# Performance work log

Measured on AMD Instinct MI355X. Metric: run time of the kernel, lower is better.

## Reference

```python
import jax, jax.numpy as jnp
import numpy as np

NUM_GRAPHS = 128
NODES_PER_GRAPH = 512
NUM_NODES = NUM_GRAPHS * NODES_PER_GRAPH
NUM_EDGES = NUM_NODES * 16
IN_DIM = 64
HID = 128
NUM_HEADS = 4
BN_EPS = 1e-5


def setup_inputs() -> dict:
    key = jax.random.key(0)
    ks = jax.random.split(key, 12)
    x = jax.random.normal(ks[0], (NUM_NODES, IN_DIM), dtype=jnp.float32)
    edge_index = jax.random.randint(ks[1], (2, NUM_EDGES), 0, NUM_NODES, dtype=jnp.int32)
    batch = jnp.repeat(jnp.arange(NUM_GRAPHS, dtype=jnp.int32), NODES_PER_GRAPH)
    s = 0.05
    W0 = jax.random.normal(ks[2], (IN_DIM, HID), dtype=jnp.float32) * s
    b0 = jnp.zeros((HID,), jnp.float32)
    Wh = jax.random.normal(ks[3], (3, HID, HID), dtype=jnp.float32) * s  # convs 1..3
    bh = jnp.zeros((3, HID), jnp.float32)
    bn_gamma = jnp.ones((4, HID), jnp.float32)
    bn_beta = jnp.zeros((4, HID), jnp.float32)
    bn_mean = jnp.zeros((4, HID), jnp.float32)
    bn_var = jnp.ones((4, HID), jnp.float32)
    attn_in_w = jax.random.normal(ks[4], (3 * HID, HID), dtype=jnp.float32) * s
    attn_in_b = jnp.zeros((3 * HID,), jnp.float32)
    attn_out_w = jax.random.normal(ks[5], (HID, HID), dtype=jnp.float32) * s
    attn_out_b = jnp.zeros((HID,), jnp.float32)
    return dict(x=x, W0=W0, b0=b0, Wh=Wh, bh=bh, bn_gamma=bn_gamma, bn_beta=bn_beta,
                bn_mean=bn_mean, bn_var=bn_var, attn_in_w=attn_in_w, attn_in_b=attn_in_b,
                attn_out_w=attn_out_w, attn_out_b=attn_out_b, edge_index=edge_index, batch=batch)


def _forward(x, W0, b0, Wh, bh, bn_gamma, bn_beta, bn_mean, bn_var,
             attn_in_w, attn_in_b, attn_out_w, attn_out_b, edge_index, batch):
    N = x.shape[0]
    src, dst = edge_index[0], edge_index[1]
    # GCN symmetric normalization with self-loops (PyG GCNConv)
    deg = jax.ops.segment_sum(jnp.ones_like(src, jnp.float32), dst, num_segments=N) + 1.0
    dis = jax.lax.rsqrt(deg)                      # deg^{-1/2}
    enorm = (dis[src] * dis[dst])[:, None]        # per-edge norm
    self_norm = (dis * dis)[:, None]              # self-loop norm

    def gcn(h, W, b):
        h = h @ W
        agg = jax.ops.segment_sum(h[src] * enorm, dst, num_segments=N)
        return agg + h * self_norm + b

    def bn(h, i):
        scale = bn_gamma[i] * jax.lax.rsqrt(bn_var[i] + BN_EPS)
        return (h - bn_mean[i]) * scale + bn_beta[i]  # eval-mode BN

    # dropout is identity in eval mode
    h = jax.nn.relu(bn(gcn(x, W0, b0), 0))
    h = jax.nn.relu(bn(gcn(h, Wh[0], bh[0]), 1))
    h = jax.nn.relu(bn(gcn(h, Wh[1], bh[1]), 2))
    f = jax.nn.relu(bn(gcn(h, Wh[2], bh[2]), 3))   # [N, HID]

    # per-graph self-attention (equal-size contiguous graphs -> batched MHA)
    dh = HID // NUM_HEADS
    xg = f.reshape(NUM_GRAPHS, NODES_PER_GRAPH, HID)
    qkv = xg @ attn_in_w.T + attn_in_b            # [G, n, 3H]
    q, k, v = jnp.split(qkv, 3, axis=-1)

    def heads(t):
        return t.reshape(NUM_GRAPHS, NODES_PER_GRAPH, NUM_HEADS, dh).transpose(0, 2, 1, 3)
    q, k, v = heads(q), heads(k), heads(v)
    scores = jnp.einsum('ghnd,ghmd->ghnm', q, k) / np.sqrt(dh).astype(np.float32)
    attn = jax.nn.softmax(scores, axis=-1)
    o = jnp.einsum('ghnm,ghmd->ghnd', attn, v).transpose(0, 2, 1, 3).reshape(NUM_GRAPHS, NODES_PER_GRAPH, HID)
    o = o @ attn_out_w.T + attn_out_b
    final = o.reshape(N, HID)

    # global mean pool over batch indices
    cnt = jax.ops.segment_sum(jnp.ones((N,), jnp.float32), batch, num_segments=NUM_GRAPHS)
    graph_emb = jax.ops.segment_sum(final, batch, num_segments=NUM_GRAPHS) / cnt[:, None]
    return final, graph_emb


def reference(x, W0, b0, Wh, bh, bn_gamma, bn_beta, bn_mean, bn_var,
              attn_in_w, attn_in_b, attn_out_w, attn_out_b, edge_index, batch):
    return _forward(x, W0, b0, Wh, bh, bn_gamma, bn_beta, bn_mean, bn_var,
                    attn_in_w, attn_in_b, attn_out_w, attn_out_b, edge_index, batch)
```

## Files before the change

### kernel.cpp

```cpp
#include <hip/hip_runtime.h>
#include <hip/hip_bf16.h>
#include <cstdint>
#include <cstddef>

#define N_NODES 65536
#define N_EDGES 1048576
#define N_GRAPHS 128
#define NPG 512
#define IN_DIM 64
#define HID 128
#define BN_EPS 1e-5f

typedef __attribute__((ext_vector_type(8))) short bf16x8;
typedef __attribute__((ext_vector_type(4))) float f32x4;
typedef __attribute__((ext_vector_type(8))) unsigned short u16x8;
typedef __attribute__((ext_vector_type(4))) unsigned int u32x4;

__device__ inline unsigned short f2bf(float f) {
  unsigned u = __builtin_bit_cast(unsigned, f);
  u = u + 0x7fffu + ((u >> 16) & 1u);
  return (unsigned short)(u >> 16);
}
__device__ inline float bf2f(unsigned short h) {
  unsigned u = ((unsigned)h) << 16;
  return __builtin_bit_cast(float, u);
}
__device__ inline void split_bf(float v, unsigned short& hi, unsigned short& lo) {
  hi = f2bf(v);
  lo = f2bf(v - bf2f(hi));
}
__device__ inline void split_bf_fast(float v, unsigned short& hi, unsigned short& lo) {
  unsigned u = __builtin_bit_cast(unsigned, v);
  hi = (unsigned short)(u >> 16);
  float r = v - __builtin_bit_cast(float, u & 0xffff0000u);
  lo = f2bf(r);
}

__global__ __launch_bounds__(256) void hist_kernel(const int* __restrict__ dst,
                                                   int* __restrict__ deg) {
  int e = blockIdx.x * 256 + threadIdx.x;
  if (e < N_EDGES) atomicAdd(&deg[dst[e]], 1);
}

__global__ __launch_bounds__(256) void dis_kernel(const int* __restrict__ deg,
                                                  float* __restrict__ dis) {
  int n = blockIdx.x * 256 + threadIdx.x;
  if (n < N_NODES) dis[n] = 1.0f / sqrtf((float)deg[n] + 1.0f);
}

__global__ __launch_bounds__(1024) void scan_kernel(const int* __restrict__ deg,
                                                    int* __restrict__ offsets,
                                                    int* __restrict__ cursor) {
  __shared__ int sums[1024];
  int t = threadIdx.x;
  int base = t * 64;
  const int4* dp = (const int4*)(deg + base);
  int s = 0;
#pragma unroll
  for (int i = 0; i < 16; i++) {
    int4 v = dp[i];
    s += v.x + v.y + v.z + v.w;
  }
  sums[t] = s;
  __syncthreads();
  for (int off = 1; off < 1024; off <<= 1) {
    int v = (t >= off) ? sums[t - off] : 0;
    __syncthreads();
    sums[t] += v;
    __syncthreads();
  }
  int run = (t == 0) ? 0 : sums[t - 1];
#pragma unroll
  for (int i = 0; i < 16; i++) {
    int4 v = dp[i];
    int idx = base + i * 4;
    offsets[idx] = run; cursor[idx] = run; run += v.x;
    offsets[idx + 1] = run; cursor[idx + 1] = run; run += v.y;
    offsets[idx + 2] = run; cursor[idx + 2] = run; run += v.z;
    offsets[idx + 3] = run; cursor[idx + 3] = run; run += v.w;
  }
  if (t == 1023) offsets[N_NODES] = run;
}

__global__ __launch_bounds__(256) void fill_kernel(const int* __restrict__ src,
                                                   const int* __restrict__ dst,
                                                   int* __restrict__ cursor,
                                                   int* __restrict__ csr) {
  int e = blockIdx.x * 256 + threadIdx.x;
  if (e < N_EDGES) {
    int d = dst[e];
    int slot = atomicAdd(&cursor[d], 1);
    csr[slot] = src[e];
  }
}

__global__ __launch_bounds__(256) void agg64_kernel(const float* __restrict__ x,
                                                    const float* __restrict__ dis,
                                                    const int* __restrict__ offsets,
                                                    const int* __restrict__ csr,
                                                    unsigned short* __restrict__ zhi,
                                                    unsigned short* __restrict__ zlo) {
  int node = blockIdx.x * 4 + (threadIdx.x >> 6);
  int lane = threadIdx.x & 63;
  float dn = dis[node];
  float acc = x[(size_t)node * 64 + lane] * dn * dn;
  int beg = offsets[node], end = offsets[node + 1];
  int k = beg;
  for (; k + 4 <= end; k += 4) {
    int s0 = csr[k], s1 = csr[k + 1], s2 = csr[k + 2], s3 = csr[k + 3];
    float w0 = dn * dis[s0], w1 = dn * dis[s1], w2 = dn * dis[s2], w3 = dn * dis[s3];
    float v0 = x[(size_t)s0 * 64 + lane];
    float v1 = x[(size_t)s1 * 64 + lane];
    float v2 = x[(size_t)s2 * 64 + lane];
    float v3 = x[(size_t)s3 * 64 + lane];
    acc = fmaf(w0, v0, acc);
    acc = fmaf(w1, v1, acc);
    acc = fmaf(w2, v2, acc);
    acc = fmaf(w3, v3, acc);
  }
  for (; k < end; k++) {
    int s = csr[k];
    acc = fmaf(dn * dis[s], x[(size_t)s * 64 + lane], acc);
  }
  unsigned short h_, l_;
  split_bf(acc, h_, l_);
  zhi[(size_t)node * 64 + lane] = h_;
  zlo[(size_t)node * 64 + lane] = l_;
}

__global__ __launch_bounds__(256) void agg128_kernel(const float* __restrict__ h,
                                                     const float* __restrict__ dis,
                                                     const int* __restrict__ offsets,
                                                     const int* __restrict__ csr,
                                                     unsigned short* __restrict__ zhi,
                                                     unsigned short* __restrict__ zlo) {
  int node = blockIdx.x * 4 + (threadIdx.x >> 6);
  int lane = threadIdx.x & 63;
  float dn = dis[node];
  float sn = dn * dn;
  const float* hr = h + (size_t)node * 128;
  float a0 = hr[lane] * sn;
  float a1 = hr[lane + 64] * sn;
  int beg = offsets[node], end = offsets[node + 1];
  int k = beg;
  for (; k + 4 <= end; k += 4) {
    int s0 = csr[k], s1 = csr[k + 1], s2 = csr[k + 2], s3 = csr[k + 3];
    float w0 = dn * dis[s0], w1 = dn * dis[s1], w2 = dn * dis[s2], w3 = dn * dis[s3];
    const float* p0 = h + (size_t)s0 * 128;
    const float* p1 = h + (size_t)s1 * 128;
    const float* p2 = h + (size_t)s2 * 128;
    const float* p3 = h + (size_t)s3 * 128;
    float u0 = p0[lane], d0 = p0[lane + 64];
    float u1 = p1[lane], d1 = p1[lane + 64];
    float u2 = p2[lane], d2 = p2[lane + 64];
    float u3 = p3[lane], d3 = p3[lane + 64];
    a0 = fmaf(w0, u0, a0); a1 = fmaf(w0, d0, a1);
    a0 = fmaf(w1, u1, a0); a1 = fmaf(w1, d1, a1);
    a0 = fmaf(w2, u2, a0); a1 = fmaf(w2, d2, a1);
    a0 = fmaf(w3, u3, a0); a1 = fmaf(w3, d3, a1);
  }
  for (; k < end; k++) {
    int s = csr[k];
    float w = dn * dis[s];
    const float* hs = h + (size_t)s * 128;
    a0 = fmaf(w, hs[lane], a0);
    a1 = fmaf(w, hs[lane + 64], a1);
  }
  unsigned short h0, l0, h1, l1;
  split_bf(a0, h0, l0);
  split_bf(a1, h1, l1);
  zhi[(size_t)node * 128 + lane] = h0;
  zlo[(size_t)node * 128 + lane] = l0;
  zhi[(size_t)node * 128 + lane + 64] = h1;
  zlo[(size_t)node * 128 + lane + 64] = l1;
}

template <bool TRANS>
__global__ __launch_bounds__(256) void wprep_kernel(const float* __restrict__ W, int K, int O,
                                                    unsigned short* __restrict__ hi,
                                                    unsigned short* __restrict__ lo) {
  int idx = blockIdx.x * 256 + threadIdx.x;
  int KC = K / 32;
  int total = (O / 16) * KC * 64;
  if (idx >= total) return;
  int lane = idx & 63;
  int rest = idx >> 6;
  int kc = rest % KC;
  int nt = rest / KC;
  int n = nt * 16 + (lane & 15);
  int kb = kc * 32 + (lane >> 4) * 8;
  unsigned short* hp = hi + (size_t)idx * 8;
  unsigned short* lp = lo + (size_t)idx * 8;
#pragma unroll
  for (int j = 0; j < 8; j++) {
    int k = kb + j;
    float v = TRANS ? W[(size_t)n * K + k] : W[(size_t)k * O + n];
    unsigned short h_, l_;
    split_bf(v, h_, l_);
    hp[j] = h_;
    lp[j] = l_;
  }
}

template <int K, int O, bool DOBN, bool DORELU, bool SPLIT_OUT, bool GROUPED,
          bool DOPOOL = false>
__global__ __launch_bounds__(256) void gemm_mfma(
    const unsigned short* __restrict__ Ahi, const unsigned short* __restrict__ Alo,
    const unsigned short* __restrict__ Whi, const unsigned short* __restrict__ Wlo,
    const float* __restrict__ bias,
    const float* __restrict__ gamma, const float* __restrict__ beta,
    const float* __restrict__ mean, const float* __restrict__ var,
    float* __restrict__ Cf, unsigned short* __restrict__ Chi,
    unsigned short* __restrict__ Clo, float* __restrict__ Pool = nullptr) {
  constexpr int KC = K / 32;
  int wave = threadIdx.x >> 6;
  int lane = threadIdx.x & 63;
  int m0 = blockIdx.x * 128 + wave * 32;
  int o0 = blockIdx.y * 128;
  int mrow = lane & 15;
  int kseg = (lane >> 4) * 8;

  f32x4 acc[2][8];
#pragma unroll
  for (int mt = 0; mt < 2; mt++)
#pragma unroll
    for (int nt = 0; nt < 8; nt++) acc[mt][nt] = (f32x4)0.0f;

#pragma unroll
  for (int kc = 0; kc < KC; kc++) {
    bf16x8 ah[2], al[2];
#pragma unroll
    for (int mt = 0; mt < 2; mt++) {
      size_t aoff = (size_t)(m0 + mt * 16 + mrow) * K + kc * 32 + kseg;
      ah[mt] = *(const bf16x8*)(Ahi + aoff);
      al[mt] = *(const bf16x8*)(Alo + aoff);
    }
#pragma unroll
    for (int nt = 0; nt < 8; nt++) {
      size_t foff = (((size_t)(blockIdx.y * 8 + nt) * KC + kc) * 64 + lane) * 8;
      bf16x8 bh = *(const bf16x8*)(Whi + foff);
      bf16x8 bl = *(const bf16x8*)(Wlo + foff);
#pragma unroll
      for (int mt = 0; mt < 2; mt++) {
        acc[mt][nt] = __builtin_amdgcn_mfma_f32_16x16x32_bf16(ah[mt], bh, acc[mt][nt], 0, 0, 0);
        acc[mt][nt] = __builtin_amdgcn_mfma_f32_16x16x32_bf16(ah[mt], bl, acc[mt][nt], 0, 0, 0);
        acc[mt][nt] = __builtin_amdgcn_mfma_f32_16x16x32_bf16(al[mt], bh, acc[mt][nt], 0, 0, 0);
        acc[mt][nt] = __builtin_amdgcn_mfma_f32_16x16x32_bf16(al[mt], bl, acc[mt][nt], 0, 0, 0);
      }
    }
  }

  int ccol = lane & 15;
  int crow0 = (lane >> 4) * 4;
  float colsum[8];
  if constexpr (DOPOOL) {
#pragma unroll
    for (int nt = 0; nt < 8; nt++) colsum[nt] = 0.0f;
  }
#pragma unroll
  for (int nt = 0; nt < 8; nt++) {
    int c = o0 + nt * 16 + ccol;
    float sc, cb;
    float b = bias[c];
    if (DOBN) {
      sc = gamma[c] * rsqrtf(var[c] + BN_EPS);
      cb = (b - mean[c]) * sc + beta[c];
    } else {
      sc = 1.0f;
      cb = b;
    }
#pragma unroll
    for (int mt = 0; mt < 2; mt++) {
#pragma unroll
      for (int r = 0; r < 4; r++) {
        float v = fmaf(acc[mt][nt][r], sc, cb);
        if (DORELU) v = fmaxf(v, 0.0f);
        size_t row = (size_t)(m0 + mt * 16 + crow0 + r);
        if (SPLIT_OUT) {
          unsigned short h_, l_;
          split_bf(v, h_, l_);
          if (GROUPED) {
            size_t base = row * (size_t)(2 * O) + (size_t)(((c >> 5) << 6) + (c & 31));
            Chi[base] = h_;
            Chi[base + 32] = l_;
          } else {
            Chi[row * O + c] = h_;
            Clo[row * O + c] = l_;
          }
        } else {
          Cf[row * O + c] = v;
        }
        if constexpr (DOPOOL) colsum[nt] += v;
      }
    }
  }
  if constexpr (DOPOOL) {
    __shared__ float pb[4][128];
#pragma unroll
    for (int nt = 0; nt < 8; nt++) {
      float cs = colsum[nt];
      cs += __shfl_xor(cs, 16, 64);
      cs += __shfl_xor(cs, 32, 64);
      if ((lane >> 4) == 0) pb[wave][nt * 16 + ccol] = cs;
    }
    __syncthreads();
    int tt = threadIdx.x;
    if (tt < 128) {
      float s2 = pb[0][tt] + pb[1][tt] + pb[2][tt] + pb[3][tt];
      int gg = blockIdx.x >> 2;
      atomicAdd(&Pool[gg * 128 + tt], s2 * (1.0f / NPG));
    }
  }
}

__global__ __launch_bounds__(256) void knorm_kernel(const unsigned short* __restrict__ qvs,
                                                    float* __restrict__ kmax2) {
  int g = blockIdx.x >> 2;
  int h = blockIdx.x & 3;
  size_t gbase = (size_t)g * NPG;
  float best = 0.0f;
#pragma unroll
  for (int r = 0; r < 2; r++) {
    int j = r * 256 + threadIdx.x;
    size_t base = (gbase + j) * 768 + (size_t)(4 + h) * 64;
    float s = 0.0f;
#pragma unroll
    for (int i = 0; i < 4; i++) {
      u16x8 hh = *(const u16x8*)(qvs + base + i * 8);
      u16x8 ll = *(const u16x8*)(qvs + base + 32 + i * 8);
#pragma unroll
      for (int jj = 0; jj < 8; jj++) {
        float v = bf2f(hh[jj]) + bf2f(ll[jj]);
        s = fmaf(v, v, s);
      }
    }
    best = fmaxf(best, s);
  }
#pragma unroll
  for (int off = 32; off >= 1; off >>= 1)
    best = fmaxf(best, __shfl_xor(best, off, 64));
  __shared__ float red[4];
  int wave = threadIdx.x >> 6;
  if ((threadIdx.x & 63) == 0) red[wave] = best;
  __syncthreads();
  if (threadIdx.x == 0) {
    float m = fmaxf(fmaxf(red[0], red[1]), fmaxf(red[2], red[3]));
    kmax2[blockIdx.x] = m;
  }
}

__global__ __launch_bounds__(256, 2) void attn_mfma_kernel(
    const unsigned short* __restrict__ qvs, const float* __restrict__ kmax2,
    unsigned short* __restrict__ ohi, unsigned short* __restrict__ olo) {
  int wb = ((blockIdx.x & 7) << 7) | (blockIdx.x >> 3);
  int g = wb >> 3;
  int h = (wb >> 1) & 3;
  int half = wb & 1;
  int t = threadIdx.x;
  int wave = t >> 6;
  int lane = t & 63;
  int quad = lane >> 4;
  int l15 = lane & 15;
  size_t gbase = (size_t)g * NPG;
  int qb = half * 256 + wave * 64;

  const float cf = 0.17677669529663687f * 1.4426950408889634f;

  __shared__ unsigned short Kh[2][32][40] __attribute__((aligned(16)));
  __shared__ unsigned short Kl[2][32][40] __attribute__((aligned(16)));
  __shared__ unsigned short Vh[2][33][40] __attribute__((aligned(16)));
  __shared__ unsigned short Vl[2][33][40] __attribute__((aligned(16)));
  __shared__ float Ot[64 * 36] __attribute__((aligned(16)));

  bf16x8 qh[4], ql[4];
  float Mq[4];
  float km2 = kmax2[g * 4 + h];
#pragma unroll
  for (int mt = 0; mt < 4; mt++) {
    size_t qoff = (gbase + qb + mt * 16 + l15) * 768 + (size_t)h * 64 + quad * 8;
    u16x8 hh = *(const u16x8*)(qvs + qoff);
    u16x8 ll = *(const u16x8*)(qvs + qoff + 32);
    qh[mt] = __builtin_bit_cast(bf16x8, hh);
    ql[mt] = __builtin_bit_cast(bf16x8, ll);
    float s = 0.0f;
#pragma unroll
    for (int j = 0; j < 8; j++) {
      float v = bf2f(hh[j]) + bf2f(ll[j]);
      s = fmaf(v, v, s);
    }
    s += __shfl_xor(s, 16);
    s += __shfl_xor(s, 32);
    Mq[mt] = cf * sqrtf(s * km2);
  }

  f32x4 Oa[4][3];
#pragma unroll
  for (int mt = 0; mt < 4; mt++)
#pragma unroll
    for (int nt = 0; nt < 3; nt++) Oa[mt][nt] = (f32x4)0.0f;

  if (t >= 64 && t < 72) {
    int u = t - 64;
    int bsel = u >> 2;
    int i = u & 3;
    u16x8 ones;
#pragma unroll
    for (int j = 0; j < 8; j++) ones[j] = 0x3F80;
    *(u16x8*)&Vh[bsel][32][i * 8] = ones;
  }

  bool isK = (t >= 128);
  bool isV = (t < 64);
  u16x8 kreg_h, kreg_l;
  ushort4 vreg_h[4], vreg_l[4];
  int kkey = 0, kds = 0, kphys = 0, vkeyb = 0, vdvb = 0;
  if (isK) {
    int t2 = t - 128;
    kkey = t2 >> 2;
    kds = (t2 & 3) * 8;
    int nt_ = kkey >> 4, q_ = (kkey >> 2) & 3, r_ = kkey & 3;
    int p_ = (nt_ << 1) | (r_ >> 1);
    kphys = 8 * (q_ ^ p_) + 2 * p_ + (r_ & 1);
  } else if (isV) {
    vkeyb = (t & 7) * 4;
    vdvb = (t >> 3) * 4;
  }

  auto load_chunk = [&](int c) {
    if (isK) {
      size_t ko = (gbase + (size_t)(c * 32 + kphys)) * 768 + (size_t)(4 + h) * 64 + kds;
      kreg_h = *(const u16x8*)(qvs + ko);
      kreg_l = *(const u16x8*)(qvs + ko + 32);
    } else if (isV) {
#pragma unroll
      for (int r = 0; r < 4; r++) {
        size_t vo = (gbase + (size_t)(c * 32 + vkeyb + r)) * 768 + (size_t)(8 + h) * 64 + vdvb;
        vreg_h[r] = *(const ushort4*)(qvs + vo);
        vreg_l[r] = *(const ushort4*)(qvs + vo + 32);
      }
    }
  };

  auto stage_chunk = [&](int bsel) {
    if (isK) {
      *(u16x8*)&Kh[bsel][kkey][kds] = kreg_h;
      *(u16x8*)&Kl[bsel][kkey][kds] = kreg_l;
    } else if (isV) {
      unsigned short ha[4][4], la[4][4];
#pragma unroll
      for (int r = 0; r < 4; r++) {
        *(ushort4*)&ha[r][0] = vreg_h[r];
        *(ushort4*)&la[r][0] = vreg_l[r];
      }
#pragma unroll
      for (int c2 = 0; c2 < 4; c2++) {
        ushort4 hv, lv;
        hv.x = ha[0][c2]; hv.y = ha[1][c2]; hv.z = ha[2][c2]; hv.w = ha[3][c2];
        lv.x = la[0][c2]; lv.y = la[1][c2]; lv.z = la[2][c2]; lv.w = la[3][c2];
        *(ushort4*)&Vh[bsel][vdvb + c2][vkeyb] = hv;
        *(ushort4*)&Vl[bsel][vdvb + c2][vkeyb] = lv;
      }
    }
  };

  load_chunk(0);
  stage_chunk(0);
  __syncthreads();

  int p = 0;
  for (int c = 0; c < 16; c++) {
    if (c < 15) load_chunk(c + 1);

    bf16x8 akh[2], akl[2];
    akh[0] = *(const bf16x8*)&Kh[p][l15][quad * 8];
    akh[1] = *(const bf16x8*)&Kh[p][16 + l15][quad * 8];
    akl[0] = *(const bf16x8*)&Kl[p][l15][quad * 8];
    akl[1] = *(const bf16x8*)&Kl[p][16 + l15][quad * 8];
    bf16x8 bvh0 = *(const bf16x8*)&Vh[p][l15][quad * 8];
    bf16x8 bvl0 = *(const bf16x8*)&Vl[p][l15][quad * 8];
    bf16x8 bvh1 = *(const bf16x8*)&Vh[p][16 + l15][quad * 8];
    bf16x8 bvl1 = *(const bf16x8*)&Vl[p][16 + l15][quad * 8];
    bf16x8 bvh2 = *(const bf16x8*)&Vh[p][32 + l15][quad * 8];

#pragma unroll
    for (int mt = 0; mt < 4; mt++) {
      unsigned pkh[4], pkl[4];
#pragma unroll
      for (int nt = 0; nt < 2; nt++) {
        f32x4 S = (f32x4)0.0f;
        S = __builtin_amdgcn_mfma_f32_16x16x32_bf16(akh[nt], qh[mt], S, 0, 0, 0);
        S = __builtin_amdgcn_mfma_f32_16x16x32_bf16(akh[nt], ql[mt], S, 0, 0, 0);
        S = __builtin_amdgcn_mfma_f32_16x16x32_bf16(akl[nt], qh[mt], S, 0, 0, 0);
        S = __builtin_amdgcn_mfma_f32_16x16x32_bf16(akl[nt], ql[mt], S, 0, 0, 0);
        unsigned short h0, l0, h1, l1, h2, l2, h3, l3;
        split_bf_fast(__builtin_exp2f(fmaf(S[0], cf, -Mq[mt])), h0, l0);
        split_bf_fast(__builtin_exp2f(fmaf(S[1], cf, -Mq[mt])), h1, l1);
        split_bf_fast(__builtin_exp2f(fmaf(S[2], cf, -Mq[mt])), h2, l2);
        split_bf_fast(__builtin_exp2f(fmaf(S[3], cf, -Mq[mt])), h3, l3);
        pkh[nt * 2]     = (unsigned)h0 | ((unsigned)h1 << 16);
        pkh[nt * 2 + 1] = (unsigned)h2 | ((unsigned)h3 << 16);
        pkl[nt * 2]     = (unsigned)l0 | ((unsigned)l1 << 16);
        pkl[nt * 2 + 1] = (unsigned)l2 | ((unsigned)l3 << 16);
      }
      u32x4 uh, ul;
      uh[0] = pkh[0];
      uh[1] = (unsigned)__shfl_xor((int)pkh[1], 16, 64);
      uh[2] = (unsigned)__shfl_xor((int)pkh[2], 32, 64);
      uh[3] = (unsigned)__shfl_xor((int)pkh[3], 48, 64);
      ul[0] = pkl[0];
      ul[1] = (unsigned)__shfl_xor((int)pkl[1], 16, 64);
      ul[2] = (unsigned)__shfl_xor((int)pkl[2], 32, 64);
      ul[3] = (unsigned)__shfl_xor((int)pkl[3], 48, 64);
      bf16x8 pa_h = __builtin_bit_cast(bf16x8, uh);
      bf16x8 pa_l = __builtin_bit_cast(bf16x8, ul);

      Oa[mt][0] = __builtin_amdgcn_mfma_f32_16x16x32_bf16(pa_h, bvh0, Oa[mt][0], 0, 0, 0);
      Oa[mt][0] = __builtin_amdgcn_mfma_f32_16x16x32_bf16(pa_h, bvl0, Oa[mt][0], 0, 0, 0);
      Oa[mt][0] = __builtin_amdgcn_mfma_f32_16x16x32_bf16(pa_l, bvh0, Oa[mt][0], 0, 0, 0);
      Oa[mt][1] = __builtin_amdgcn_mfma_f32_16x16x32_bf16(pa_h, bvh1, Oa[mt][1], 0, 0, 0);
      Oa[mt][1] = __builtin_amdgcn_mfma_f32_16x16x32_bf16(pa_h, bvl1, Oa[mt][1], 0, 0, 0);
      Oa[mt][1] = __builtin_amdgcn_mfma_f32_16x16x32_bf16(pa_l, bvh1, Oa[mt][1], 0, 0, 0);
      Oa[mt][2] = __builtin_amdgcn_mfma_f32_16x16x32_bf16(pa_h, bvh2, Oa[mt][2], 0, 0, 0);
      Oa[mt][2] = __builtin_amdgcn_mfma_f32_16x16x32_bf16(pa_l, bvh2, Oa[mt][2], 0, 0, 0);
    }

    if (c < 15) stage_chunk(p ^ 1);
    __syncthreads();
    p ^= 1;
  }

  for (int w = 0; w < 4; w++) {
    if (wave == w) {
#pragma unroll
      for (int mt = 0; mt < 4; mt++) {
#pragma unroll
        for (int r = 0; r < 4; r++) {
          int row = mt * 16 + quad * 4 + r;
          Ot[row * 36 + l15] = Oa[mt][0][r];
          Ot[row * 36 + 16 + l15] = Oa[mt][1][r];
          if (l15 == 0) Ot[row * 36 + 32] = Oa[mt][2][r];
        }
      }
      int row = lane;
      float inv = 1.0f / Ot[row * 36 + 32];
      size_t node = gbase + qb + row;
      u16x8 vh, vl;
#pragma unroll
      for (int seg = 0; seg < 4; seg++) {
#pragma unroll
        for (int j = 0; j < 8; j++) {
          unsigned short hi_, lo_;
          split_bf_fast(Ot[row * 36 + seg * 8 + j] * inv, hi_, lo_);
          vh[j] = hi_;
          vl[j] = lo_;
        }
        *(u16x8*)(ohi + node * 128 + h * 32 + seg * 8) = vh;
        *(u16x8*)(olo + node * 128 + h * 32 + seg * 8) = vl;
      }
    }
    __syncthreads();
  }
}

extern "C" void kernel_launch(void* const* d_in, const int* in_sizes, int n_in,
                              void* d_out, int out_size, void* d_ws, size_t ws_size,
                              hipStream_t stream) {
  (void)in_sizes; (void)n_in; (void)out_size; (void)ws_size;
  const float* x          = (const float*)d_in[0];
  const float* W0         = (const float*)d_in[1];
  const float* b0         = (const float*)d_in[2];
  const float* Wh         = (const float*)d_in[3];
  const float* bh         = (const float*)d_in[4];
  const float* bn_gamma   = (const float*)d_in[5];
  const float* bn_beta    = (const float*)d_in[6];
  const float* bn_mean    = (const float*)d_in[7];
  const float* bn_var     = (const float*)d_in[8];
  const float* attn_in_w  = (const float*)d_in[9];
  const float* attn_in_b  = (const float*)d_in[10];
  const float* attn_out_w = (const float*)d_in[11];
  const float* attn_out_b = (const float*)d_in[12];
  const int* edge_index   = (const int*)d_in[13];
  const int* src = edge_index;
  const int* dst = edge_index + N_EDGES;

  char* ws = (char*)d_ws;
  size_t off = 0;
  auto alloc = [&](size_t bytes) -> void* {
    void* p = ws + off;
    off += (bytes + 255) & ~(size_t)255;
    return p;
  };
  int*   deg     = (int*)alloc((size_t)N_NODES * 4);
  int*   offsets = (int*)alloc((size_t)(N_NODES + 1) * 4);
  int*   cursor  = (int*)alloc((size_t)N_NODES * 4);
  int*   csr     = (int*)alloc((size_t)N_EDGES * 4);
  float* dis     = (float*)alloc((size_t)N_NODES * 4);
  float* bufA    = (float*)alloc((size_t)N_NODES * HID * 4);
  unsigned short* zhi = (unsigned short*)alloc((size_t)N_NODES * HID * 2);
  unsigned short* zlo = (unsigned short*)alloc((size_t)N_NODES * HID * 2);
  unsigned short* qvs = (unsigned short*)alloc((size_t)N_NODES * 768 * 2);
  float* kmax2   = (float*)alloc((size_t)N_GRAPHS * 4 * 4);
  unsigned short* w0h = (unsigned short*)alloc(8192 * 2);
  unsigned short* w0l = (unsigned short*)alloc(8192 * 2);
  unsigned short* whh[3], *whl[3];
  for (int i = 0; i < 3; i++) {
    whh[i] = (unsigned short*)alloc(16384 * 2);
    whl[i] = (unsigned short*)alloc(16384 * 2);
  }
  unsigned short* wqh = (unsigned short*)alloc(49152 * 2);
  unsigned short* wql = (unsigned short*)alloc(49152 * 2);
  unsigned short* woh = (unsigned short*)alloc(16384 * 2);
  unsigned short* wol = (unsigned short*)alloc(16384 * 2);

  unsigned short* fhi = (unsigned short*)bufA;
  unsigned short* flo = fhi + (size_t)N_NODES * HID;

  float* fin = (float*)d_out;
  float* emb = fin + (size_t)N_NODES * HID;

  hipMemsetAsync(deg, 0, (size_t)N_NODES * 4, stream);
  hipMemsetAsync(emb, 0, (size_t)N_GRAPHS * HID * 4, stream);
  hist_kernel<<<N_EDGES / 256, 256, 0, stream>>>(dst, deg);
  dis_kernel<<<N_NODES / 256, 256, 0, stream>>>(deg, dis);
  scan_kernel<<<1, 1024, 0, stream>>>(deg, offsets, cursor);
  fill_kernel<<<N_EDGES / 256, 256, 0, stream>>>(src, dst, cursor, csr);

  wprep_kernel<false><<<4, 256, 0, stream>>>(W0, 64, 128, w0h, w0l);
  for (int i = 0; i < 3; i++)
    wprep_kernel<false><<<8, 256, 0, stream>>>(Wh + (size_t)i * HID * HID, 128, 128,
                                               whh[i], whl[i]);
  wprep_kernel<true><<<24, 256, 0, stream>>>(attn_in_w, 128, 384, wqh, wql);
  wprep_kernel<true><<<8, 256, 0, stream>>>(attn_out_w, 128, 128, woh, wol);

  dim3 ggrid(N_NODES / 128, 1);
  agg64_kernel<<<N_NODES / 4, 256, 0, stream>>>(x, dis, offsets, csr, zhi, zlo);
  gemm_mfma<64, 128, true, true, false, false><<<ggrid, 256, 0, stream>>>(
      zhi, zlo, w0h, w0l, b0, bn_gamma, bn_beta, bn_mean, bn_var, bufA, nullptr, nullptr);
  for (int L = 0; L < 2; L++) {
    agg128_kernel<<<N_NODES / 4, 256, 0, stream>>>(bufA, dis, offsets, csr, zhi, zlo);
    gemm_mfma<128, 128, true, true, false, false><<<ggrid, 256, 0, stream>>>(
        zhi, zlo, whh[L], whl[L], bh + (size_t)L * HID,
        bn_gamma + (size_t)(L + 1) * HID, bn_beta + (size_t)(L + 1) * HID,
        bn_mean + (size_t)(L + 1) * HID, bn_var + (size_t)(L + 1) * HID,
        bufA, nullptr, nullptr);
  }
  agg128_kernel<<<N_NODES / 4, 256, 0, stream>>>(bufA, dis, offsets, csr, zhi, zlo);
  gemm_mfma<128, 128, true, true, true, false><<<ggrid, 256, 0, stream>>>(
      zhi, zlo, whh[2], whl[2], bh + (size_t)2 * HID,
      bn_gamma + (size_t)3 * HID, bn_beta + (size_t)3 * HID,
      bn_mean + (size_t)3 * HID, bn_var + (size_t)3 * HID,
      nullptr, fhi, flo);
  dim3 qgrid(N_NODES / 128, 3);
  gemm_mfma<128, 384, false, false, true, true><<<qgrid, 256, 0, stream>>>(
      fhi, flo, wqh, wql, attn_in_b, nullptr, nullptr, nullptr, nullptr,
      nullptr, qvs, nullptr);
  knorm_kernel<<<N_GRAPHS * 4, 256, 0, stream>>>(qvs, kmax2);
  attn_mfma_kernel<<<N_GRAPHS * 4 * 2, 256, 0, stream>>>(qvs, kmax2, zhi, zlo);
  gemm_mfma<128, 128, false, false, false, false, true><<<ggrid, 256, 0, stream>>>(
      zhi, zlo, woh, wol, attn_out_b, nullptr, nullptr, nullptr, nullptr,
      fin, nullptr, nullptr, emb);
}
```

Measured before the change: 806.2 us.

## Unroll edge gathers by eight, use packed bf16 converts, precompute chunk pointers

```diff
diff --git a/kernel.cpp b/kernel.cpp
--- a/kernel.cpp
+++ b/kernel.cpp
@@ -34,6 +34,17 @@
   hi = (unsigned short)(u >> 16);
   float r = v - __builtin_bit_cast(float, u & 0xffff0000u);
   lo = f2bf(r);
+}
+__device__ inline unsigned cvt_pk_bf16(float a, float b) {
+  unsigned r;
+  asm("v_cvt_pk_bf16_f32 %0, %1, %2" : "=v"(r) : "v"(a), "v"(b));
+  return r;
+}
+__device__ inline void split2_pk(float a, float b, unsigned& hpk, unsigned& lpk) {
+  hpk = cvt_pk_bf16(a, b);
+  float ha = __builtin_bit_cast(float, hpk << 16);
+  float hb = __builtin_bit_cast(float, hpk & 0xffff0000u);
+  lpk = cvt_pk_bf16(a - ha, b - hb);
 }
 
 __global__ __launch_bounds__(256) void hist_kernel(const int* __restrict__ dst,
@@ -106,17 +117,18 @@
   float acc = x[(size_t)node * 64 + lane] * dn * dn;
   int beg = offsets[node], end = offsets[node + 1];
   int k = beg;
-  for (; k + 4 <= end; k += 4) {
-    int s0 = csr[k], s1 = csr[k + 1], s2 = csr[k + 2], s3 = csr[k + 3];
-    float w0 = dn * dis[s0], w1 = dn * dis[s1], w2 = dn * dis[s2], w3 = dn * dis[s3];
-    float v0 = x[(size_t)s0 * 64 + lane];
-    float v1 = x[(size_t)s1 * 64 + lane];
-    float v2 = x[(size_t)s2 * 64 + lane];
-    float v3 = x[(size_t)s3 * 64 + lane];
-    acc = fmaf(w0, v0, acc);
-    acc = fmaf(w1, v1, acc);
-    acc = fmaf(w2, v2, acc);
-    acc = fmaf(w3, v3, acc);
+  for (; k + 8 <= end; k += 8) {
+    int s[8];
+#pragma unroll
+    for (int i = 0; i < 8; i++) s[i] = csr[k + i];
+    float w[8];
+#pragma unroll
+    for (int i = 0; i < 8; i++) w[i] = dn * dis[s[i]];
+    float v[8];
+#pragma unroll
+    for (int i = 0; i < 8; i++) v[i] = x[(size_t)s[i] * 64 + lane];
+#pragma unroll
+    for (int i = 0; i < 8; i++) acc = fmaf(w[i], v[i], acc);
   }
   for (; k < end; k++) {
     int s = csr[k];
@@ -143,21 +155,25 @@
   float a1 = hr[lane + 64] * sn;
   int beg = offsets[node], end = offsets[node + 1];
   int k = beg;
-  for (; k + 4 <= end; k += 4) {
-    int s0 = csr[k], s1 = csr[k + 1], s2 = csr[k + 2], s3 = csr[k + 3];
-    float w0 = dn * dis[s0], w1 = dn * dis[s1], w2 = dn * dis[s2], w3 = dn * dis[s3];
-    const float* p0 = h + (size_t)s0 * 128;
-    const float* p1 = h + (size_t)s1 * 128;
-    const float* p2 = h + (size_t)s2 * 128;
-    const float* p3 = h + (size_t)s3 * 128;
-    float u0 = p0[lane], d0 = p0[lane + 64];
-    float u1 = p1[lane], d1 = p1[lane + 64];
-    float u2 = p2[lane], d2 = p2[lane + 64];
-    float u3 = p3[lane], d3 = p3[lane + 64];
-    a0 = fmaf(w0, u0, a0); a1 = fmaf(w0, d0, a1);
-    a0 = fmaf(w1, u1, a0); a1 = fmaf(w1, d1, a1);
-    a0 = fmaf(w2, u2, a0); a1 = fmaf(w2, d2, a1);
-    a0 = fmaf(w3, u3, a0); a1 = fmaf(w3, d3, a1);
+  for (; k + 8 <= end; k += 8) {
+    int s[8];
+#pragma unroll
+    for (int i = 0; i < 8; i++) s[i] = csr[k + i];
+    float w[8];
+#pragma unroll
+    for (int i = 0; i < 8; i++) w[i] = dn * dis[s[i]];
+    float u[8], d[8];
+#pragma unroll
+    for (int i = 0; i < 8; i++) {
+      const float* p = h + (size_t)s[i] * 128;
+      u[i] = p[lane];
+      d[i] = p[lane + 64];
+    }
+#pragma unroll
+    for (int i = 0; i < 8; i++) {
+      a0 = fmaf(w[i], u[i], a0);
+      a1 = fmaf(w[i], d[i], a1);
+    }
   }
   for (; k < end; k++) {
     int s = csr[k];
@@ -413,36 +429,42 @@
   bool isV = (t < 64);
   u16x8 kreg_h, kreg_l;
   ushort4 vreg_h[4], vreg_l[4];
-  int kkey = 0, kds = 0, kphys = 0, vkeyb = 0, vdvb = 0;
+  int kkey = 0, vkeyb = 0, vdvb = 0;
+  const unsigned short* kptr = nullptr;
+  const unsigned short* vptr = nullptr;
+  const size_t CSTRIDE = (size_t)32 * 768;
   if (isK) {
     int t2 = t - 128;
     kkey = t2 >> 2;
-    kds = (t2 & 3) * 8;
+    int kds = (t2 & 3) * 8;
     int nt_ = kkey >> 4, q_ = (kkey >> 2) & 3, r_ = kkey & 3;
     int p_ = (nt_ << 1) | (r_ >> 1);
-    kphys = 8 * (q_ ^ p_) + 2 * p_ + (r_ & 1);
+    int kphys = 8 * (q_ ^ p_) + 2 * p_ + (r_ & 1);
+    kptr = qvs + (gbase + (size_t)kphys) * 768 + (size_t)(4 + h) * 64 + kds;
   } else if (isV) {
     vkeyb = (t & 7) * 4;
     vdvb = (t >> 3) * 4;
-  }
-
-  auto load_chunk = [&](int c) {
+    vptr = qvs + (gbase + (size_t)vkeyb) * 768 + (size_t)(8 + h) * 64 + vdvb;
+  }
+
+  auto load_chunk = [&]() {
     if (isK) {
-      size_t ko = (gbase + (size_t)(c * 32 + kphys)) * 768 + (size_t)(4 + h) * 64 + kds;
-      kreg_h = *(const u16x8*)(qvs + ko);
-      kreg_l = *(const u16x8*)(qvs + ko + 32);
+      kreg_h = *(const u16x8*)kptr;
+      kreg_l = *(const u16x8*)(kptr + 32);
+      kptr += CSTRIDE;
     } else if (isV) {
 #pragma unroll
       for (int r = 0; r < 4; r++) {
-        size_t vo = (gbase + (size_t)(c * 32 + vkeyb + r)) * 768 + (size_t)(8 + h) * 64 + vdvb;
-        vreg_h[r] = *(const ushort4*)(qvs + vo);
-        vreg_l[r] = *(const ushort4*)(qvs + vo + 32);
-      }
+        vreg_h[r] = *(const ushort4*)(vptr + (size_t)r * 768);
+        vreg_l[r] = *(const ushort4*)(vptr + (size_t)r * 768 + 32);
+      }
+      vptr += CSTRIDE;
     }
   };
 
   auto stage_chunk = [&](int bsel) {
     if (isK) {
+      int kds = ((t - 128) & 3) * 8;
       *(u16x8*)&Kh[bsel][kkey][kds] = kreg_h;
       *(u16x8*)&Kl[bsel][kkey][kds] = kreg_l;
     } else if (isV) {
@@ -463,13 +485,13 @@
     }
   };
 
-  load_chunk(0);
+  load_chunk();
   stage_chunk(0);
   __syncthreads();
 
   int p = 0;
   for (int c = 0; c < 16; c++) {
-    if (c < 15) load_chunk(c + 1);
+    if (c < 15) load_chunk();
 
     bf16x8 akh[2], akl[2];
     akh[0] = *(const bf16x8*)&Kh[p][l15][quad * 8];
@@ -492,15 +514,12 @@
         S = __builtin_amdgcn_mfma_f32_16x16x32_bf16(akh[nt], ql[mt], S, 0, 0, 0);
         S = __builtin_amdgcn_mfma_f32_16x16x32_bf16(akl[nt], qh[mt], S, 0, 0, 0);
         S = __builtin_amdgcn_mfma_f32_16x16x32_bf16(akl[nt], ql[mt], S, 0, 0, 0);
-        unsigned short h0, l0, h1, l1, h2, l2, h3, l3;
-        split_bf_fast(__builtin_exp2f(fmaf(S[0], cf, -Mq[mt])), h0, l0);
-        split_bf_fast(__builtin_exp2f(fmaf(S[1], cf, -Mq[mt])), h1, l1);
-        split_bf_fast(__builtin_exp2f(fmaf(S[2], cf, -Mq[mt])), h2, l2);
-        split_bf_fast(__builtin_exp2f(fmaf(S[3], cf, -Mq[mt])), h3, l3);
-        pkh[nt * 2]     = (unsigned)h0 | ((unsigned)h1 << 16);
-        pkh[nt * 2 + 1] = (unsigned)h2 | ((unsigned)h3 << 16);
-        pkl[nt * 2]     = (unsigned)l0 | ((unsigned)l1 << 16);
-        pkl[nt * 2 + 1] = (unsigned)l2 | ((unsigned)l3 << 16);
+        float p0 = __builtin_exp2f(fmaf(S[0], cf, -Mq[mt]));
+        float p1 = __builtin_exp2f(fmaf(S[1], cf, -Mq[mt]));
+        float p2 = __builtin_exp2f(fmaf(S[2], cf, -Mq[mt]));
+        float p3 = __builtin_exp2f(fmaf(S[3], cf, -Mq[mt]));
+        split2_pk(p0, p1, pkh[nt * 2], pkl[nt * 2]);
+        split2_pk(p2, p3, pkh[nt * 2 + 1], pkl[nt * 2 + 1]);
       }
       u32x4 uh, ul;
       uh[0] = pkh[0];
@@ -544,18 +563,26 @@
       int row = lane;
       float inv = 1.0f / Ot[row * 36 + 32];
       size_t node = gbase + qb + row;
-      u16x8 vh, vl;
 #pragma unroll
       for (int seg = 0; seg < 4; seg++) {
-#pragma unroll
-        for (int j = 0; j < 8; j++) {
-          unsigned short hi_, lo_;
-          split_bf_fast(Ot[row * 36 + seg * 8 + j] * inv, hi_, lo_);
-          vh[j] = hi_;
-          vl[j] = lo_;
-        }
-        *(u16x8*)(ohi + node * 128 + h * 32 + seg * 8) = vh;
-        *(u16x8*)(olo + node * 128 + h * 32 + seg * 8) = vl;
+        float v0 = Ot[row * 36 + seg * 8 + 0] * inv;
+        float v1 = Ot[row * 36 + seg * 8 + 1] * inv;
+        float v2 = Ot[row * 36 + seg * 8 + 2] * inv;
+        float v3 = Ot[row * 36 + seg * 8 + 3] * inv;
+        float v4 = Ot[row * 36 + seg * 8 + 4] * inv;
+        float v5 = Ot[row * 36 + seg * 8 + 5] * inv;
+        float v6 = Ot[row * 36 + seg * 8 + 6] * inv;
+        float v7 = Ot[row * 36 + seg * 8 + 7] * inv;
+        unsigned h0, l0, h1, l1, h2, l2, h3, l3;
+        split2_pk(v0, v1, h0, l0);
+        split2_pk(v2, v3, h1, l1);
+        split2_pk(v4, v5, h2, l2);
+        split2_pk(v6, v7, h3, l3);
+        u32x4 hw, lw;
+        hw[0] = h0; hw[1] = h1; hw[2] = h2; hw[3] = h3;
+        lw[0] = l0; lw[1] = l1; lw[2] = l2; lw[3] = l3;
+        *(u32x4*)(ohi + node * 128 + h * 32 + seg * 8) = hw;
+        *(u32x4*)(olo + node * 128 + h * 32 + seg * 8) = lw;
       }
     }
     __syncthreads();
```

New measurement: 807.9 us. No clear change (+0.2%).
